# Optimization experiments

Measured on AMD Instinct MI355X. Metric: run time of the kernel, lower is better.

The kernel has to match this reference:

```python
import jax, jax.numpy as jnp
import numpy as np

N, M, D = 16384, 1024, 32


def setup_inputs() -> dict:
    key = jax.random.key(0)
    k1, k2 = jax.random.split(key)
    x = jax.random.normal(k1, (N, D), dtype=jnp.float32)
    centers = jax.random.normal(k2, (M, D), dtype=jnp.float32)
    sigma = jnp.ones((M, D), dtype=jnp.float32)  # get_sigma_ones(s=1.0)
    return {"x": x, "centers": centers, "sigma": sigma}


def reference(x, centers, sigma):
    # Gaussian RBF kernel: exp(-0.5 * delta^T invCov delta) / sqrt((2pi)^D det(S))
    d = x.shape[1]
    s2 = sigma ** 2  # (M, D)
    # invCovMat: inverse of per-center diagonal covariance -> diag(1/s2)
    invCov = jnp.eye(d, dtype=x.dtype) * (1.0 / s2)[:, :, None]  # (M, D, D)
    # denom: sqrt((2pi)^D * prod(s2))
    k = (2.0 * np.pi) ** d  # python float, safe for D=32 in f32
    detS = jnp.sqrt(jnp.asarray(k, x.dtype) * jnp.prod(s2, axis=1))  # (M,)
    delta = x[:, None, :] - centers[None, :, :]  # (N, M, D)
    # batched (1,D) @ (D,D) per (n,m) pair, then elementwise * delta and reduce
    q = jnp.einsum('nmd,mde->nme', delta, invCov)  # (N, M, D)
    X = jnp.sum(q * delta, axis=2)  # (N, M) squared Mahalanobis distance
    return jnp.exp(-0.5 * X) / detS[None, :]  # (N, M)
```

## Files before the change

kernel.cpp:

```cpp
#include <hip/hip_runtime.h>


#define N_  16384
#define M_  1024
#define D_  32
#define NT  32
#define BLK 256

typedef float v4f __attribute__((ext_vector_type(4)));
#define PIN(v) asm volatile("" : "+v"(v))

#define L2E_      1.4426950408889634f
#define LOG2_2PI_ 2.6514961294723187f

#define WS_NEED (8 * M_ * 16 + 4 * M_ * 4)

__global__ __launch_bounds__(64) void rbf_pre(
    const float* __restrict__ centers, const float* __restrict__ sigma,
    v4f* __restrict__ At, float* __restrict__ qc, float* __restrict__ c0f,
    float* __restrict__ g0, float* __restrict__ flag)
{
    const int m = blockIdx.x * 64 + threadIdx.x;
    const v4f* cg = (const v4f*)(centers + (size_t)m * D_);
    const v4f* sg = (const v4f*)(sigma   + (size_t)m * D_);

    v4f cv[8], s2v[8];
    #pragma unroll
    for (int j = 0; j < 8; ++j) {
        cv[j] = cg[j];
        v4f s = sg[j];
        s2v[j] = s * s;
    }
    const float s2_0 = s2v[0].x;
    bool uf = true;
    float pr = 1.0f;
    #pragma unroll
    for (int j = 0; j < 8; ++j) {
        #pragma unroll
        for (int e = 0; e < 4; ++e) {
            float v = s2v[j][e];
            uf = uf && (v == s2_0);
            pr *= v;
        }
    }
    const float ld = log2f(pr);

    const float w0 = 1.0f / s2_0;
    float b = 0.f;
    #pragma unroll
    for (int j = 0; j < 8; ++j) {
        v4f a = cv[j] * w0;
        At[(size_t)j * M_ + m] = a;
        b = fmaf(cv[j].x, a.x, b);
        b = fmaf(cv[j].y, a.y, b);
        b = fmaf(cv[j].z, a.z, b);
        b = fmaf(cv[j].w, a.w, b);
    }
    const float g = -0.5f * (D_ * LOG2_2PI_ + ld);
    g0[m]   = g;
    c0f[m]  = fmaf(-0.5f * L2E_, b, g);
    qc[m]   = -0.5f * L2E_ * w0;
    flag[m] = uf ? 1.0f : 0.0f;
}

__global__ __launch_bounds__(BLK, 6) void rbf_main(
    const float* __restrict__ x, const float* __restrict__ centers,
    const float* __restrict__ sigma, float* __restrict__ out,
    const v4f* __restrict__ At, const float* __restrict__ qc,
    const float* __restrict__ c0f, const float* __restrict__ g0,
    const float* __restrict__ flag)
{
    const int tid = threadIdx.x;
    const int m   = blockIdx.x * BLK + tid;
    const int n0  = blockIdx.y * NT;

    __shared__ __align__(16) float r2s[NT];

    {
        const v4f* xg = (const v4f*)(x + (size_t)n0 * D_);
        v4f v = xg[tid];
        float s = fmaf(v.x, v.x, fmaf(v.y, v.y, fmaf(v.z, v.z, v.w * v.w)));
        s += __shfl_xor(s, 1);
        s += __shfl_xor(s, 2);
        s += __shfl_xor(s, 4);
        if ((tid & 7) == 0) r2s[tid >> 3] = s;
    }
    __syncthreads();

    const float fl = flag[m];
    if (__all(fl != 0.0f)) {
        const float qcm = qc[m];
        const float c0m = c0f[m];
        v4f A[8];
        #pragma unroll
        for (int j = 0; j < 8; ++j) A[j] = At[(size_t)j * M_ + m];
        #pragma unroll
        for (int j = 0; j < 8; ++j) PIN(A[j]);

        const v4f* r2v = (const v4f*)r2s;
        float* o0 = out + (size_t)n0 * M_ + m;

        #pragma unroll 1
        for (int i = 0; i < NT; i += 8) {
            v4f ra = r2v[i / 4];
            v4f rb = r2v[i / 4 + 1];
            #pragma unroll
            for (int k = 0; k < 8; ++k) {
                const v4f* row = (const v4f*)(x + (size_t)(n0 + i + k) * D_);
                v4f x0 = row[0], x1 = row[1], x2 = row[2], x3 = row[3];
                v4f x4 = row[4], x5 = row[5], x6 = row[6], x7 = row[7];
                v4f p = x0 * A[0];
                v4f q = x1 * A[1];
                p += x2 * A[2];  q += x3 * A[3];
                p += x4 * A[4];  q += x5 * A[5];
                p += x6 * A[6];  q += x7 * A[7];
                v4f t = p + q;
                float dot = (t.x + t.y) + (t.z + t.w);
                float rr  = (k < 4) ? ra[k] : rb[k - 4];
                float f   = fmaf(L2E_, dot, fmaf(qcm, rr, c0m));
                __builtin_nontemporal_store(__builtin_amdgcn_exp2f(f),
                                            o0 + (size_t)(i + k) * M_);
            }
        }
    } else {
        const float c0 = g0[m];
        const float* cg = centers + (size_t)m * D_;
        const float* sg = sigma   + (size_t)m * D_;
        #pragma unroll 1
        for (int i = 0; i < NT; ++i) {
            const float* xr = x + (size_t)(n0 + i) * D_;
            float a0 = 0.f, a1 = 0.f;
            #pragma unroll
            for (int d = 0; d < D_; d += 2) {
                float s0 = sg[d], s1 = sg[d + 1];
                float t0 = xr[d]     - cg[d];
                float t1 = xr[d + 1] - cg[d + 1];
                a0 = fmaf(t0 * (1.0f / (s0 * s0)), t0, a0);
                a1 = fmaf(t1 * (1.0f / (s1 * s1)), t1, a1);
            }
            float f = fmaf(-0.5f * L2E_, a0 + a1, c0);
            out[(size_t)(n0 + i) * M_ + m] = __builtin_amdgcn_exp2f(f);
        }
    }
}

__global__ __launch_bounds__(BLK, 6) void rbf_mono(
    const float* __restrict__ x, const float* __restrict__ centers,
    const float* __restrict__ sigma, float* __restrict__ out)
{
    const int tid = threadIdx.x;
    const int m   = blockIdx.x * BLK + tid;
    const int n0  = blockIdx.y * NT;

    __shared__ __align__(16) float r2s[NT];
    {
        const v4f* xg = (const v4f*)(x + (size_t)n0 * D_);
        v4f v = xg[tid];
        float s = fmaf(v.x, v.x, fmaf(v.y, v.y, fmaf(v.z, v.z, v.w * v.w)));
        s += __shfl_xor(s, 1);
        s += __shfl_xor(s, 2);
        s += __shfl_xor(s, 4);
        if ((tid & 7) == 0) r2s[tid >> 3] = s;
    }
    __syncthreads();

    float s2_0 = 0.f, ld = 0.f;
    bool uf = true;
    {
        const float* sg = sigma + (size_t)m * D_;
        #pragma unroll
        for (int d = 0; d < D_; ++d) {
            float s  = sg[d];
            float s2 = s * s;
            if (d == 0) s2_0 = s2;
            uf = uf && (s2 == s2_0);
            ld += log2f(s2);
        }
    }

    if (__all((int)uf)) {
        const float w0 = 1.0f / s2_0;
        v4f A[8];
        float b = 0.f;
        {
            const v4f* cg = (const v4f*)(centers + (size_t)m * D_);
            #pragma unroll
            for (int j = 0; j < 8; ++j) {
                v4f c = cg[j];
                v4f a = c * w0;
                A[j] = a;
                b = fmaf(c.x, a.x, b); b = fmaf(c.y, a.y, b);
                b = fmaf(c.z, a.z, b); b = fmaf(c.w, a.w, b);
            }
        }
        #pragma unroll
        for (int j = 0; j < 8; ++j) PIN(A[j]);

        const float c0 = fmaf(-0.5f * L2E_, b, -0.5f * (D_ * LOG2_2PI_ + ld));
        const float qc = -0.5f * L2E_ * w0;
        const v4f* r2v = (const v4f*)r2s;
        float* o0 = out + (size_t)n0 * M_ + m;

        #pragma unroll 1
        for (int i = 0; i < NT; i += 8) {
            v4f ra = r2v[i / 4];
            v4f rb = r2v[i / 4 + 1];
            #pragma unroll
            for (int k = 0; k < 8; ++k) {
                const v4f* row = (const v4f*)(x + (size_t)(n0 + i + k) * D_);
                v4f x0 = row[0], x1 = row[1], x2 = row[2], x3 = row[3];
                v4f x4 = row[4], x5 = row[5], x6 = row[6], x7 = row[7];
                v4f p = x0 * A[0];
                v4f q = x1 * A[1];
                p += x2 * A[2];  q += x3 * A[3];
                p += x4 * A[4];  q += x5 * A[5];
                p += x6 * A[6];  q += x7 * A[7];
                v4f t = p + q;
                float dot = (t.x + t.y) + (t.z + t.w);
                float rr  = (k < 4) ? ra[k] : rb[k - 4];
                float f   = fmaf(L2E_, dot, fmaf(qc, rr, c0));
                __builtin_nontemporal_store(__builtin_amdgcn_exp2f(f),
                                            o0 + (size_t)(i + k) * M_);
            }
        }
    } else {
        const float c0 = -0.5f * (D_ * LOG2_2PI_ + ld);
        const float* cg = centers + (size_t)m * D_;
        const float* sg = sigma   + (size_t)m * D_;
        #pragma unroll 1
        for (int i = 0; i < NT; ++i) {
            const float* xr = x + (size_t)(n0 + i) * D_;
            float a0 = 0.f, a1 = 0.f;
            #pragma unroll
            for (int d = 0; d < D_; d += 2) {
                float s0 = sg[d], s1 = sg[d + 1];
                float t0 = xr[d]     - cg[d];
                float t1 = xr[d + 1] - cg[d + 1];
                a0 = fmaf(t0 * (1.0f / (s0 * s0)), t0, a0);
                a1 = fmaf(t1 * (1.0f / (s1 * s1)), t1, a1);
            }
            float f = fmaf(-0.5f * L2E_, a0 + a1, c0);
            out[(size_t)(n0 + i) * M_ + m] = __builtin_amdgcn_exp2f(f);
        }
    }
}

extern "C" void kernel_launch(void* const* d_in, const int* in_sizes, int n_in,
                              void* d_out, int out_size, void* d_ws, size_t ws_size,
                              hipStream_t stream) {
    const float* x = (const float*)d_in[0];
    const float* c = (const float*)d_in[1];
    const float* s = (const float*)d_in[2];
    float* out = (float*)d_out;

    if (ws_size >= (size_t)WS_NEED && d_ws != nullptr) {
        char*  w    = (char*)d_ws;
        v4f*   At   = (v4f*)w;
        float* qc   = (float*)(w + 8 * M_ * 16);
        float* c0f  = qc  + M_;
        float* g0   = c0f + M_;
        float* flag = g0  + M_;
        rbf_pre<<<dim3(M_ / 64), 64, 0, stream>>>(c, s, At, qc, c0f, g0, flag);
        dim3 grid(M_ / BLK, N_ / NT);
        rbf_main<<<grid, BLK, 0, stream>>>(x, c, s, out, At, qc, c0f, g0, flag);
    } else {
        dim3 grid(M_ / BLK, N_ / NT);
        rbf_mono<<<grid, BLK, 0, stream>>>(x, c, s, out);
    }
}
```

Measured before the change: 90.42 us.

## Process two centers per thread and stage x tile in LDS

Each thread in rbf_main now handles two centers (m0 and m0+256), so each block covers 512 centers and the grid halves in x. The x tile for the block is copied into shared memory and read from there, with each x row reused across both centers' A vectors instead of being loaded from global memory per row. The launch-bounds occupancy hint drops from 6 to 4 to make room for the extra registers, and the inner loop is restructured to walk one row at a time. The fallback mono kernel gets the same row-loop restructuring; the trade-off is fewer blocks and more register pressure per thread.

```diff
diff --git a/kernel.cpp b/kernel.cpp
--- a/kernel.cpp
+++ b/kernel.cpp
@@ -6,6 +6,7 @@
 #define D_  32
 #define NT  32
 #define BLK 256
+#define MB  512
 
 typedef float v4f __attribute__((ext_vector_type(4)));
 #define PIN(v) asm volatile("" : "+v"(v))
@@ -63,7 +64,7 @@
     flag[m] = uf ? 1.0f : 0.0f;
 }
 
-__global__ __launch_bounds__(BLK, 6) void rbf_main(
+__global__ __launch_bounds__(BLK, 4) void rbf_main(
     const float* __restrict__ x, const float* __restrict__ centers,
     const float* __restrict__ sigma, float* __restrict__ out,
     const v4f* __restrict__ At, const float* __restrict__ qc,
@@ -71,14 +72,17 @@
     const float* __restrict__ flag)
 {
     const int tid = threadIdx.x;
-    const int m   = blockIdx.x * BLK + tid;
+    const int m0  = blockIdx.x * MB + tid;
+    const int m1  = m0 + BLK;
     const int n0  = blockIdx.y * NT;
 
+    __shared__ __align__(16) v4f   xsv[NT * D_ / 4];
     __shared__ __align__(16) float r2s[NT];
 
     {
         const v4f* xg = (const v4f*)(x + (size_t)n0 * D_);
         v4f v = xg[tid];
+        xsv[tid] = v;
         float s = fmaf(v.x, v.x, fmaf(v.y, v.y, fmaf(v.z, v.z, v.w * v.w)));
         s += __shfl_xor(s, 1);
         s += __shfl_xor(s, 2);
@@ -87,59 +91,69 @@
     }
     __syncthreads();
 
-    const float fl = flag[m];
-    if (__all(fl != 0.0f)) {
-        const float qcm = qc[m];
-        const float c0m = c0f[m];
-        v4f A[8];
-        #pragma unroll
-        for (int j = 0; j < 8; ++j) A[j] = At[(size_t)j * M_ + m];
-        #pragma unroll
-        for (int j = 0; j < 8; ++j) PIN(A[j]);
-
-        const v4f* r2v = (const v4f*)r2s;
-        float* o0 = out + (size_t)n0 * M_ + m;
-
-        #pragma unroll 1
-        for (int i = 0; i < NT; i += 8) {
-            v4f ra = r2v[i / 4];
-            v4f rb = r2v[i / 4 + 1];
-            #pragma unroll
-            for (int k = 0; k < 8; ++k) {
-                const v4f* row = (const v4f*)(x + (size_t)(n0 + i + k) * D_);
-                v4f x0 = row[0], x1 = row[1], x2 = row[2], x3 = row[3];
-                v4f x4 = row[4], x5 = row[5], x6 = row[6], x7 = row[7];
-                v4f p = x0 * A[0];
-                v4f q = x1 * A[1];
-                p += x2 * A[2];  q += x3 * A[3];
-                p += x4 * A[4];  q += x5 * A[5];
-                p += x6 * A[6];  q += x7 * A[7];
-                v4f t = p + q;
-                float dot = (t.x + t.y) + (t.z + t.w);
-                float rr  = (k < 4) ? ra[k] : rb[k - 4];
-                float f   = fmaf(L2E_, dot, fmaf(qcm, rr, c0m));
-                __builtin_nontemporal_store(__builtin_amdgcn_exp2f(f),
-                                            o0 + (size_t)(i + k) * M_);
-            }
+    const bool fl = (flag[m0] != 0.0f) && (flag[m1] != 0.0f);
+    if (__all((int)fl)) {
+        const float qc0 = qc[m0],  qc1 = qc[m1];
+        const float c00 = c0f[m0], c01 = c0f[m1];
+        v4f A[8], B[8];
+        #pragma unroll
+        for (int j = 0; j < 8; ++j) {
+            A[j] = At[(size_t)j * M_ + m0];
+            B[j] = At[(size_t)j * M_ + m1];
+        }
+        #pragma unroll
+        for (int j = 0; j < 8; ++j) { PIN(A[j]); PIN(B[j]); }
+
+        float* o0 = out + (size_t)n0 * M_ + m0;
+
+        #pragma unroll 1
+        for (int i = 0; i < NT; ++i) {
+            const v4f* row = xsv + i * 8;
+            v4f p0 = {0,0,0,0}, q0 = {0,0,0,0};
+            v4f p1 = {0,0,0,0}, q1 = {0,0,0,0};
+            #pragma unroll
+            for (int j = 0; j < 8; j += 2) {
+                v4f xa = row[j];
+                v4f xb = row[j + 1];
+                p0 += xa * A[j];
+                q0 += xb * A[j + 1];
+                p1 += xa * B[j];
+                q1 += xb * B[j + 1];
+            }
+            float rr = r2s[i];
+            v4f t0 = p0 + q0;
+            v4f t1 = p1 + q1;
+            float d0 = (t0.x + t0.y) + (t0.z + t0.w);
+            float d1 = (t1.x + t1.y) + (t1.z + t1.w);
+            float f0 = fmaf(L2E_, d0, fmaf(qc0, rr, c00));
+            float f1 = fmaf(L2E_, d1, fmaf(qc1, rr, c01));
+            __builtin_nontemporal_store(__builtin_amdgcn_exp2f(f0),
+                                        o0 + (size_t)i * M_);
+            __builtin_nontemporal_store(__builtin_amdgcn_exp2f(f1),
+                                        o0 + (size_t)i * M_ + BLK);
         }
     } else {
-        const float c0 = g0[m];
-        const float* cg = centers + (size_t)m * D_;
-        const float* sg = sigma   + (size_t)m * D_;
-        #pragma unroll 1
-        for (int i = 0; i < NT; ++i) {
-            const float* xr = x + (size_t)(n0 + i) * D_;
-            float a0 = 0.f, a1 = 0.f;
-            #pragma unroll
-            for (int d = 0; d < D_; d += 2) {
-                float s0 = sg[d], s1 = sg[d + 1];
-                float t0 = xr[d]     - cg[d];
-                float t1 = xr[d + 1] - cg[d + 1];
-                a0 = fmaf(t0 * (1.0f / (s0 * s0)), t0, a0);
-                a1 = fmaf(t1 * (1.0f / (s1 * s1)), t1, a1);
-            }
-            float f = fmaf(-0.5f * L2E_, a0 + a1, c0);
-            out[(size_t)(n0 + i) * M_ + m] = __builtin_amdgcn_exp2f(f);
+        #pragma unroll 1
+        for (int h = 0; h < 2; ++h) {
+            const int mm = (h == 0) ? m0 : m1;
+            const float c0 = g0[mm];
+            const float* cg = centers + (size_t)mm * D_;
+            const float* sg = sigma   + (size_t)mm * D_;
+            #pragma unroll 1
+            for (int i = 0; i < NT; ++i) {
+                const float* xr = (const float*)(xsv) + (size_t)i * D_;
+                float a0 = 0.f, a1 = 0.f;
+                #pragma unroll
+                for (int d = 0; d < D_; d += 2) {
+                    float s0 = sg[d], s1 = sg[d + 1];
+                    float t0 = xr[d]     - cg[d];
+                    float t1 = xr[d + 1] - cg[d + 1];
+                    a0 = fmaf(t0 * (1.0f / (s0 * s0)), t0, a0);
+                    a1 = fmaf(t1 * (1.0f / (s1 * s1)), t1, a1);
+                }
+                float f = fmaf(-0.5f * L2E_, a0 + a1, c0);
+                out[(size_t)(n0 + i) * M_ + mm] = __builtin_amdgcn_exp2f(f);
+            }
         }
     }
 }
@@ -198,30 +212,22 @@
 
         const float c0 = fmaf(-0.5f * L2E_, b, -0.5f * (D_ * LOG2_2PI_ + ld));
         const float qc = -0.5f * L2E_ * w0;
-        const v4f* r2v = (const v4f*)r2s;
         float* o0 = out + (size_t)n0 * M_ + m;
 
         #pragma unroll 1
-        for (int i = 0; i < NT; i += 8) {
-            v4f ra = r2v[i / 4];
-            v4f rb = r2v[i / 4 + 1];
-            #pragma unroll
-            for (int k = 0; k < 8; ++k) {
-                const v4f* row = (const v4f*)(x + (size_t)(n0 + i + k) * D_);
-                v4f x0 = row[0], x1 = row[1], x2 = row[2], x3 = row[3];
-                v4f x4 = row[4], x5 = row[5], x6 = row[6], x7 = row[7];
-                v4f p = x0 * A[0];
-                v4f q = x1 * A[1];
-                p += x2 * A[2];  q += x3 * A[3];
-                p += x4 * A[4];  q += x5 * A[5];
-                p += x6 * A[6];  q += x7 * A[7];
-                v4f t = p + q;
-                float dot = (t.x + t.y) + (t.z + t.w);
-                float rr  = (k < 4) ? ra[k] : rb[k - 4];
-                float f   = fmaf(L2E_, dot, fmaf(qc, rr, c0));
-                __builtin_nontemporal_store(__builtin_amdgcn_exp2f(f),
-                                            o0 + (size_t)(i + k) * M_);
-            }
+        for (int i = 0; i < NT; ++i) {
+            const v4f* row = (const v4f*)(x + (size_t)(n0 + i) * D_);
+            v4f p = {0,0,0,0}, q = {0,0,0,0};
+            #pragma unroll
+            for (int j = 0; j < 8; j += 2) {
+                p += row[j]     * A[j];
+                q += row[j + 1] * A[j + 1];
+            }
+            v4f t = p + q;
+            float dot = (t.x + t.y) + (t.z + t.w);
+            float f   = fmaf(L2E_, dot, fmaf(qc, r2s[i], c0));
+            __builtin_nontemporal_store(__builtin_amdgcn_exp2f(f),
+                                        o0 + (size_t)i * M_);
         }
     } else {
         const float c0 = -0.5f * (D_ * LOG2_2PI_ + ld);
@@ -261,7 +267,7 @@
         float* g0   = c0f + M_;
         float* flag = g0  + M_;
         rbf_pre<<<dim3(M_ / 64), 64, 0, stream>>>(c, s, At, qc, c0f, g0, flag);
-        dim3 grid(M_ / BLK, N_ / NT);
+        dim3 grid(M_ / MB, N_ / NT);
         rbf_main<<<grid, BLK, 0, stream>>>(x, c, s, out, At, qc, c0f, g0, flag);
     } else {
         dim3 grid(M_ / BLK, N_ / NT);
```

Result: slower. 93.87 us (+3.8%).
